# Performance work log

Hardware: AMD Instinct MI355X
Metric: run time of the kernel (lower is better)

Reference implementation:

```python
import jax, jax.numpy as jnp
import numpy as np

B, N, DIM = 4, 1024, 1024
H, DH = 16, 64
NUM_MEM = 4
TOPK = 64
QK_SCALE = 10.0  # qk_norm_scale


def l2norm(t, eps=1e-12):
    # qk_norm_groups == 1 -> normalize over full head dim
    return t / jnp.clip(jnp.linalg.norm(t, axis=-1, keepdims=True), eps)


def setup_inputs() -> dict:
    key = jax.random.key(0)
    ks = jax.random.split(key, 12)
    s = 0.02
    inp = {
        "x": jax.random.normal(ks[0], (B, N, DIM), dtype=jnp.float32),
        "Wq": jax.random.normal(ks[1], (DIM, H * DH), dtype=jnp.float32) * s,
        "Wk": jax.random.normal(ks[2], (DIM, H * DH), dtype=jnp.float32) * s,
        "Wv": jax.random.normal(ks[3], (DIM, H * DH), dtype=jnp.float32) * s,
        "W_pre_th": jax.random.normal(ks[4], (H, H), dtype=jnp.float32) * (1.0 / H) ** 0.5,
        "W_post_th": jax.random.normal(ks[5], (H, H), dtype=jnp.float32) * (1.0 / H) ** 0.5,
        "mem_k": jax.random.normal(ks[6], (H, NUM_MEM, DH), dtype=jnp.float32),
        "mem_v": jax.random.normal(ks[7], (H, NUM_MEM, DH), dtype=jnp.float32),
        "head_scale_params": jnp.ones((1, H, 1, 1), dtype=jnp.float32),
        "Wg": jax.random.normal(ks[8], (DIM, H * DH), dtype=jnp.float32) * s,
        "bg": jnp.ones((H * DH,), dtype=jnp.float32),
        "Wo": jax.random.normal(ks[9], (H * DH, DIM), dtype=jnp.float32) * s,
    }
    return inp


def reference(x, Wq, Wk, Wv, W_pre_th, W_post_th, mem_k, mem_v,
              head_scale_params, Wg, bg, Wo):
    b, n, _ = x.shape
    # projections -> b h n d
    q = (x @ Wq).reshape(b, n, H, DH).transpose(0, 2, 1, 3)
    k = (x @ Wk).reshape(b, n, H, DH).transpose(0, 2, 1, 3)
    v = (x @ Wv).reshape(b, n, H, DH).transpose(0, 2, 1, 3)

    # memory key/values prepended along the key axis
    mk = jnp.broadcast_to(mem_k[None], (b, H, NUM_MEM, DH))
    mv = jnp.broadcast_to(mem_v[None], (b, H, NUM_MEM, DH))
    k = jnp.concatenate([mk, k], axis=2)
    v = jnp.concatenate([mv, v], axis=2)

    # qk-norm: l2 normalize then fixed scale
    q = l2norm(q)
    k = l2norm(k)

    dots = jnp.einsum("bhid,bhjd->bhij", q, k) * QK_SCALE  # b h n (n+m)
    # pre-softmax talking heads (1x1 conv over head channels)
    dots = jnp.einsum("hg,bgij->bhij", W_pre_th, dots)

    mask_value = -jnp.finfo(dots.dtype).max
    j = n + NUM_MEM
    # causal mask, left-padded False over the memory columns
    col_pos = jnp.arange(j) - NUM_MEM  # mem cols get negative pos -> never masked
    causal = jnp.arange(n)[:, None] < col_pos[None, :]  # (n, j)
    dots = jnp.where(causal[None, None], mask_value, dots)

    # sparse top-k: keep only entries >= k-th largest per row
    top = jax.lax.top_k(dots, TOPK)[0]
    vk = top[..., -1:]
    dots = jnp.where(dots < vk, mask_value, dots)

    attn = jax.nn.softmax(dots, axis=-1)
    # post-softmax talking heads
    attn = jnp.einsum("hg,bgij->bhij", W_post_th, attn)

    out = jnp.einsum("bhij,bhjd->bhid", attn, v)
    out = out * head_scale_params
    out = out.transpose(0, 2, 1, 3).reshape(b, n, H * DH)

    gates = x @ Wg + bg
    out = out * jax.nn.sigmoid(gates)
    return out @ Wo
```

## Files before the change

### kernel.cpp

```cpp
#include <hip/hip_runtime.h>
#include <hip/hip_bf16.h>
#include <float.h>

#define B_ 4
#define N_ 1024
#define H_ 16
#define DH_ 64
#define NM_ 4
#define J_ 1028
#define IT_ 4
#define JST 1064
#define TOPK_ 64
#define QKSCALE 10.0f
#define KTF_BG 67584
#define VTF_DC 16896

typedef __attribute__((ext_vector_type(8))) short short8;
typedef __attribute__((ext_vector_type(4))) float f32x4;
typedef __attribute__((ext_vector_type(8))) unsigned short ushort8;
typedef __attribute__((ext_vector_type(4))) unsigned int u32x4;
typedef __attribute__((ext_vector_type(2))) unsigned int u32x2;
typedef _Float16 half8 __attribute__((ext_vector_type(8)));

__device__ __forceinline__ unsigned short f2b(float f){
  union { float f; unsigned int i; } c; c.f = f;
  unsigned int r = c.i + 0x7FFFu + ((c.i >> 16) & 1u);
  return (unsigned short)(r >> 16);
}
__device__ __forceinline__ unsigned short f2h(float f){
  return __builtin_bit_cast(unsigned short, (_Float16)f);
}
__device__ __forceinline__ float h2f(unsigned short u){
  return (float)__builtin_bit_cast(_Float16, u);
}
__device__ __forceinline__ unsigned int h2key(unsigned int u){
  return (u & 0x8000u) ? (~u & 0xFFFFu) : (u | 0x8000u);
}
__device__ __forceinline__ float key2f(unsigned int k){
  unsigned int u = (k & 0x8000u) ? (k & 0x7FFFu) : (~k & 0xFFFFu);
  return h2f((unsigned short)u);
}

__global__ void k_cvtAll(const float* __restrict__ x,  const float* __restrict__ wq,
                         const float* __restrict__ wk, const float* __restrict__ wv,
                         const float* __restrict__ wg, const float* __restrict__ wo,
                         unsigned short* __restrict__ xb, unsigned short* __restrict__ wcat,
                         unsigned short* __restrict__ wob,
                         const float* __restrict__ mk, const float* __restrict__ mv,
                         unsigned short* __restrict__ ktF, unsigned short* __restrict__ vtF){
  const int NX = 4096 * 1024, NW = 1024 * 1024;
  if (blockIdx.x >= 2044){
    int h = (blockIdx.x - 2044) * 4 + (threadIdx.x >> 6);
    int d = threadIdx.x & 63;
    unsigned short kh[4], vh[4];
    #pragma unroll
    for (int mm = 0; mm < 4; ++mm){
      float kv = mk[(h * 4 + mm) * 64 + d];
      float ss = kv * kv;
      #pragma unroll
      for (int off = 32; off; off >>= 1) ss += __shfl_xor(ss, off);
      kh[mm] = f2h(kv / fmaxf(sqrtf(ss), 1e-12f));
      vh[mm] = f2h(mv[(h * 4 + mm) * 64 + d]);
    }
    for (int b = 0; b < B_; ++b){
      int bg = b * 16 + h;
      #pragma unroll
      for (int mm = 0; mm < 4; ++mm)
        ktF[(size_t)bg * KTF_BG + (size_t)(d >> 5) * 512 + (mm + ((d >> 3) & 3) * 16) * 8 + (d & 7)] = kh[mm];
      #pragma unroll
      for (int mm = 0; mm < 4; ++mm)
        vtF[(size_t)bg * KTF_BG + (size_t)(d >> 4) * VTF_DC + (d & 15) * 8 + mm] = vh[mm];
      {
        unsigned int* kz = (unsigned int*)(ktF + (size_t)bg * KTF_BG + 64 * 1024);
        for (int c = d; c < 1024; c += 64) kz[c] = 0u;
      }
      #pragma unroll
      for (int dc = 0; dc < 4; ++dc){
        unsigned int* vz = (unsigned int*)(vtF + (size_t)bg * KTF_BG + (size_t)dc * VTF_DC + 32 * 512);
        for (int c = d; c < 256; c += 64) vz[c] = 0u;
      }
    }
    return;
  }
  int i = blockIdx.x * 256 + threadIdx.x;
  const int st = 2044 * 256;
  for (; i < NX + 5 * NW; i += st){
    if (i < NX){ xb[i] = f2b(x[i]); }
    else {
      int k = i - NX;
      int which = k >> 20, off = k & (NW - 1);
      if (which == 4){ wob[off] = f2b(wo[off]); }
      else {
        const float* s = which == 0 ? wq : which == 1 ? wk : which == 2 ? wv : wg;
        wcat[(size_t)(off >> 10) * 4096 + which * 1024 + (off & 1023)] = f2b(s[off]);
      }
    }
  }
}

__global__ __launch_bounds__(256) void k_gemmF(const unsigned short* __restrict__ A,
                                               const unsigned short* __restrict__ Wc,
                                               unsigned short* __restrict__ qn,
                                               unsigned short* __restrict__ ktF,
                                               unsigned short* __restrict__ vtF,
                                               unsigned short* __restrict__ gate,
                                               const float* __restrict__ bgv)
{
  __shared__ unsigned short As[128][72];
  __shared__ unsigned short Bs[64][72];
  const int t = threadIdx.x;
  const int m0 = blockIdx.y * 128, n0 = blockIdx.x * 64;
  const int l = t & 63, w = t >> 6;
  const int l15 = l & 15, l4 = l >> 4;

  f32x4 acc[2][4];
  #pragma unroll
  for (int a = 0; a < 2; ++a)
    #pragma unroll
    for (int b2 = 0; b2 < 4; ++b2) acc[a][b2] = (f32x4){0.f, 0.f, 0.f, 0.f};

  for (int k0 = 0; k0 < 1024; k0 += 64){
    #pragma unroll
    for (int cc = 0; cc < 4; ++cc){
      int c = t + cc * 256;
      int row = c >> 3, colc = (c & 7) * 8;
      *(ushort8*)&As[row][colc] = *(const ushort8*)&A[(m0 + row) * 1024 + k0 + colc];
    }
    #pragma unroll
    for (int cc = 0; cc < 2; ++cc){
      int c = t + cc * 256;
      int kk = c >> 3, nc = (c & 7) * 8;
      ushort8 vb = *(const ushort8*)&Wc[(size_t)(k0 + kk) * 4096 + n0 + nc];
      #pragma unroll
      for (int e = 0; e < 8; ++e) Bs[nc + e][kk] = vb[e];
    }
    __syncthreads();
    #pragma unroll
    for (int ks = 0; ks < 64; ks += 32){
      short8 af[2], bfr[4];
      #pragma unroll
      for (int mf = 0; mf < 2; ++mf) af[mf]  = *(const short8*)&As[w * 32 + mf * 16 + l15][ks + l4 * 8];
      #pragma unroll
      for (int nf = 0; nf < 4; ++nf) bfr[nf] = *(const short8*)&Bs[nf * 16 + l15][ks + l4 * 8];
      #pragma unroll
      for (int mf = 0; mf < 2; ++mf)
        #pragma unroll
        for (int nf = 0; nf < 4; ++nf)
          acc[mf][nf] = __builtin_amdgcn_mfma_f32_16x16x32_bf16(af[mf], bfr[nf], acc[mf][nf], 0, 0, 0);
    }
    __syncthreads();
  }

  const int which = n0 >> 10;
  const int ncol0 = n0 & 1023;
  const int hcol = ncol0 >> 6;
  #pragma unroll
  for (int mf = 0; mf < 2; ++mf){
    if (which == 2){
      int row0 = m0 + w * 32 + mf * 16 + l4 * 4;
      int bb = row0 >> 10;
      int j0 = (row0 & 1023) + NM_;
      int jtE = j0 >> 5, lj = (j0 & 31) >> 3, e0 = j0 & 7;
      #pragma unroll
      for (int nf = 0; nf < 4; ++nf){
        int col = ncol0 + nf * 16 + l15;
        int h = col >> 6, d = col & 63;
        unsigned int lo = (unsigned int)f2h(acc[mf][nf][0]) | ((unsigned int)f2h(acc[mf][nf][1]) << 16);
        unsigned int hi = (unsigned int)f2h(acc[mf][nf][2]) | ((unsigned int)f2h(acc[mf][nf][3]) << 16);
        unsigned short* dst = vtF + (size_t)(bb * 16 + h) * KTF_BG +
                              (size_t)(d >> 4) * VTF_DC + (size_t)jtE * 512 +
                              ((d & 15) + lj * 16) * 8 + e0;
        *(u32x2*)dst = (u32x2){lo, hi};
      }
    } else {
      #pragma unroll
      for (int r = 0; r < 4; ++r){
        int row = m0 + w * 32 + mf * 16 + l4 * 4 + r;
        float rn = 1.f;
        if (which <= 1){
          float ss = 0.f;
          #pragma unroll
          for (int nf = 0; nf < 4; ++nf) ss += acc[mf][nf][r] * acc[mf][nf][r];
          #pragma unroll
          for (int off = 1; off < 16; off <<= 1) ss += __shfl_xor(ss, off);
          rn = 1.f / fmaxf(sqrtf(ss), 1e-12f);
          if (which == 0) rn *= QKSCALE;
        }
        #pragma unroll
        for (int nf = 0; nf < 4; ++nf){
          int col = ncol0 + nf * 16 + l15;
          float v = acc[mf][nf][r];
          int bb = row >> 10, ii = row & 1023;
          if (which == 3){
            float g = v + bgv[3 * 1024 + col];
            gate[(size_t)row * 1024 + col] = f2h(1.f / (1.f + __expf(-g)));
          } else if (which == 0){
            int d = col & 63;
            qn[((size_t)(bb * H_ + hcol) * N_ + ii) * DH_ + d] = f2h(v * rn);
          } else {
            int j = ii + NM_;
            int d = col & 63;
            ktF[(size_t)(bb * 16 + hcol) * KTF_BG + (size_t)(j >> 4) * 1024 +
                (size_t)(d >> 5) * 512 + ((j & 15) + ((d >> 3) & 3) * 16) * 8 + (d & 7)]
              = f2h(v * rn);
          }
        }
      }
    }
  }
}

__global__ __launch_bounds__(256) void k_gemmO(const unsigned short* __restrict__ A,
                                               const unsigned short* __restrict__ W,
                                               float* __restrict__ outp)
{
  __shared__ unsigned short As[128][72];
  __shared__ unsigned short Bs[64][72];
  const int t = threadIdx.x;
  const int m0 = blockIdx.y * 128, n0 = blockIdx.x * 64;
  const int l = t & 63, w = t >> 6;
  const int l15 = l & 15, l4 = l >> 4;

  f32x4 acc[2][4];
  #pragma unroll
  for (int a = 0; a < 2; ++a)
    #pragma unroll
    for (int b2 = 0; b2 < 4; ++b2) acc[a][b2] = (f32x4){0.f, 0.f, 0.f, 0.f};

  for (int k0 = 0; k0 < 1024; k0 += 64){
    #pragma unroll
    for (int cc = 0; cc < 4; ++cc){
      int c = t + cc * 256;
      int row = c >> 3, colc = (c & 7) * 8;
      *(ushort8*)&As[row][colc] = *(const ushort8*)&A[(m0 + row) * 1024 + k0 + colc];
    }
    #pragma unroll
    for (int cc = 0; cc < 2; ++cc){
      int c = t + cc * 256;
      int kk = c >> 3, nc = (c & 7) * 8;
      ushort8 vb = *(const ushort8*)&W[(size_t)(k0 + kk) * 1024 + n0 + nc];
      #pragma unroll
      for (int e = 0; e < 8; ++e) Bs[nc + e][kk] = vb[e];
    }
    __syncthreads();
    #pragma unroll
    for (int ks = 0; ks < 64; ks += 32){
      short8 af[2], bfr[4];
      #pragma unroll
      for (int mf = 0; mf < 2; ++mf) af[mf]  = *(const short8*)&As[w * 32 + mf * 16 + l15][ks + l4 * 8];
      #pragma unroll
      for (int nf = 0; nf < 4; ++nf) bfr[nf] = *(const short8*)&Bs[nf * 16 + l15][ks + l4 * 8];
      #pragma unroll
      for (int mf = 0; mf < 2; ++mf)
        #pragma unroll
        for (int nf = 0; nf < 4; ++nf)
          acc[mf][nf] = __builtin_amdgcn_mfma_f32_16x16x32_bf16(af[mf], bfr[nf], acc[mf][nf], 0, 0, 0);
    }
    __syncthreads();
  }

  #pragma unroll
  for (int mf = 0; mf < 2; ++mf)
    #pragma unroll
    for (int r = 0; r < 4; ++r){
      int row = m0 + w * 32 + mf * 16 + l4 * 4 + r;
      #pragma unroll
      for (int nf = 0; nf < 4; ++nf)
        outp[(size_t)row * 1024 + n0 + nf * 16 + l15] = acc[mf][nf][r];
    }
}

__global__ __launch_bounds__(1024) void k_attnM(
  const unsigned short* __restrict__ qn, const unsigned short* __restrict__ ktF,
  const unsigned short* __restrict__ vtF, const float* __restrict__ wpre,
  const float* __restrict__ wpost, const float* __restrict__ hsc,
  const unsigned short* __restrict__ gate, unsigned short* __restrict__ aout)
{
  __shared__ unsigned short sd[16 * IT_ * JST];
  __shared__ unsigned short qls[16 * 4 * 64];
  __shared__ unsigned short wpre16[16 * 32];
  __shared__ unsigned short wpost16[16 * 32];

  const int blk = blockIdx.x;
  const int b = (blk >> 1) & 3;
  const int idx = ((blk >> 3) << 1) | (blk & 1);
  const int rd = idx >> 6, jj = idx & 63;
  const int it = (rd == 0) ? (255 - jj) : (rd == 1) ? (128 + jj) : (rd == 2) ? (127 - jj) : jj;
  const int i0 = it * IT_;
  const int nAmax = i0 + IT_ + 4;
  const int nJtA = (nAmax + 15) >> 4;
  const int nJtE = (nAmax + 31) >> 5;
  const int nJtD = nJtE * 2;
  const int jc = nJtE * 32;
  const int t = threadIdx.x;
  const int w = t >> 6, l = t & 63;
  const int l15 = l & 15, l4 = l >> 4;

  if (t < 256){
    int h = t >> 4, g = t & 15;
    wpre16[h * 32 + g]       = f2h(wpre[h * 16 + g]);
    wpre16[h * 32 + 16 + g]  = 0;
    wpost16[h * 32 + g]      = f2h(wpost[h * 16 + g]);
    wpost16[h * 32 + 16 + g] = 0;
  }
  for (int c = t; c < 2048; c += 1024){
    int d2 = c & 31, ii = (c >> 5) & 3, g = c >> 7;
    ((unsigned int*)qls)[c] =
      *(const unsigned int*)(qn + ((size_t)(b * 16 + g) * N_ + i0 + ii) * 64 + d2 * 2);
  }
  __syncthreads();

  {
    const int nw16 = (nJtA > w) ? ((nJtA - w + 15) >> 4) : 0;
    const int ntask = nw16 * 16;
    if (ntask > 0){
      const int tmax = ntask - 1;
      const unsigned short* kl = ktF + (size_t)(b * 16) * KTF_BG + (size_t)l * 8;
      auto kp = [&](int task)->const unsigned short*{
        int tt = task > tmax ? tmax : task;
        int g = tt & 15, jti = tt >> 4;
        return kl + (size_t)g * KTF_BG + (((size_t)(w + jti * 16)) << 10);
      };
      const unsigned short* p0 = kp(0);
      const unsigned short* p1 = kp(1);
      half8 kA0 = *(const half8*)p0, kA1 = *(const half8*)(p0 + 512);
      half8 kB0 = *(const half8*)p1, kB1 = *(const half8*)(p1 + 512);
      for (int task = 0; task < ntask; task += 2){
        half8 cA0 = kA0, cA1 = kA1, cB0 = kB0, cB1 = kB1;
        const unsigned short* pa = kp(task + 2);
        const unsigned short* pb = kp(task + 3);
        kA0 = *(const half8*)pa; kA1 = *(const half8*)(pa + 512);
        kB0 = *(const half8*)pb; kB1 = *(const half8*)(pb + 512);
        #pragma unroll
        for (int s = 0; s < 2; ++s){
          const int tt = task + s;
          const int g = tt & 15, jt = w + ((tt >> 4) << 4);
          const unsigned short* qp = &qls[(g * 4 + (l15 & 3)) * 64 + l4 * 8];
          half8 qf0 = *(const half8*)(qp);
          half8 qf1 = *(const half8*)(qp + 32);
          f32x4 acc = (f32x4){0.f, 0.f, 0.f, 0.f};
          acc = __builtin_amdgcn_mfma_f32_16x16x32_f16(s ? cB0 : cA0, qf0, acc, 0, 0, 0);
          acc = __builtin_amdgcn_mfma_f32_16x16x32_f16(s ? cB1 : cA1, qf1, acc, 0, 0, 0);
          if (l15 < IT_){
            unsigned int pk0 = (unsigned int)f2h(acc[0]) | ((unsigned int)f2h(acc[1]) << 16);
            unsigned int pk1 = (unsigned int)f2h(acc[2]) | ((unsigned int)f2h(acc[3]) << 16);
            unsigned int* dst = (unsigned int*)&sd[(g * IT_ + l15) * JST + jt * 16 + l4 * 4];
            dst[0] = pk0; dst[1] = pk1;
          }
        }
      }
    }
  }
  __syncthreads();

  {
    half8 wa = *(const half8*)&wpre16[l15 * 32 + l4 * 8];
    const int ntask = IT_ * nJtA;
    for (int task = w; task < ntask; task += 16){
      const int ii = task & (IT_ - 1), jt = task >> 2;
      unsigned int fb[4] = {0u, 0u, 0u, 0u};
      if (l4 < 2){
        const unsigned short* src = &sd[((l4 * 8) * IT_ + ii) * JST + jt * 16 + l15];
        #pragma unroll
        for (int e = 0; e < 8; e += 2){
          unsigned int lo = src[(size_t)(e)     * IT_ * JST];
          unsigned int hi = src[(size_t)(e + 1) * IT_ * JST];
          fb[e >> 1] = (lo & 0xFFFFu) | (hi << 16);
        }
      }
      f32x4 acc = (f32x4){0.f, 0.f, 0.f, 0.f};
      acc = __builtin_amdgcn_mfma_f32_16x16x32_f16(wa, __builtin_bit_cast(half8, *(u32x4*)fb), acc, 0, 0, 0);
      #pragma unroll
      for (int r = 0; r < 4; ++r)
        sd[((l4 * 4 + r) * IT_ + ii) * JST + jt * 16 + l15] = f2h(acc[r]);
    }
  }
  __syncthreads();

  for (int rr = 0; rr < 4; ++rr){
    const int row = w * 4 + rr;
    const int g = row >> 2, ii = row & 3;
    const int nA = i0 + ii + 5;
    unsigned short* rowp = &sd[(g * IT_ + ii) * JST];
    unsigned int kw[9];
    #pragma unroll
    for (int grp = 0; grp < 9; ++grp){
      kw[grp] = 0u;
      if (grp * 128 < jc){
        int j = grp * 128 + l * 2;
        unsigned int u = (j < JST) ? *(const unsigned int*)(rowp + j) : 0u;
        unsigned int klo = h2key(u & 0xFFFFu);
        unsigned int khi = h2key(u >> 16);
        if (j     >= nA) klo = 0u;
        if (j + 1 >= nA) khi = 0u;
        kw[grp] = klo | (khi << 16);
      }
    }
    unsigned int kmx = 0u;
    #pragma unroll
    for (int grp = 0; grp < 9; ++grp){
      if (grp * 128 < jc){
        unsigned int m2 = max(kw[grp] >> 16, kw[grp] & 0xFFFFu);
        kmx = max(kmx, m2);
      }
    }
    #pragma unroll
    for (int off = 32; off; off >>= 1) kmx = max(kmx, (unsigned int)__shfl_xor((int)kmx, off));
    const float mx = key2f(kmx);

    unsigned int T = 0u;
    if (nA > TOPK_){
      for (int bit = 15; bit >= 2; --bit){
        unsigned int Tc = T | (1u << bit);
        int c = 0;
        #pragma unroll
        for (int grp = 0; grp < 9; ++grp){
          if (grp * 128 < jc){
            c += __popcll(__ballot((kw[grp] & 0xFFFFu) >= Tc));
            c += __popcll(__ballot((kw[grp] >> 16) >= Tc));
          }
        }
        if (c >= TOPK_){
          T = Tc;
          if (c == TOPK_) break;
        }
      }
    }
    if (T == 0u) T = 1u;

    float s = 0.f;
    float ev[18];
    #pragma unroll
    for (int grp = 0; grp < 9; ++grp){
      if (grp * 128 < jc){
        unsigned int klo = kw[grp] & 0xFFFFu, khi = kw[grp] >> 16;
        float elo = (klo >= T) ? __expf(key2f(klo) - mx) : 0.f;
        float ehi = (khi >= T) ? __expf(key2f(khi) - mx) : 0.f;
        ev[grp * 2] = elo; ev[grp * 2 + 1] = ehi;
        s += elo + ehi;
      }
    }
    #pragma unroll
    for (int off = 32; off; off >>= 1) s += __shfl_xor(s, off);
    float inv = 1.f / s;
    #pragma unroll
    for (int grp = 0; grp < 9; ++grp){
      if (grp * 128 < jc){
        int j = grp * 128 + l * 2;
        if (j < JST)
          *(unsigned int*)(rowp + j) =
            (unsigned int)f2h(ev[grp * 2] * inv) | ((unsigned int)f2h(ev[grp * 2 + 1] * inv) << 16);
      }
    }
  }
  __syncthreads();

  {
    const int ntask = IT_ * nJtD;
    for (int task = w; task < ntask; task += 16){
      const int ii = task & (IT_ - 1), jt = task >> 2;
      half8 wa = *(const half8*)&wpost16[l15 * 32 + l4 * 8];
      unsigned int fb[4] = {0u, 0u, 0u, 0u};
      if (l4 < 2){
        const unsigned short* src = &sd[((l4 * 8) * IT_ + ii) * JST + jt * 16 + l15];
        #pragma unroll
        for (int e = 0; e < 8; e += 2){
          unsigned int lo = src[(size_t)(e)     * IT_ * JST];
          unsigned int hi = src[(size_t)(e + 1) * IT_ * JST];
          fb[e >> 1] = (lo & 0xFFFFu) | (hi << 16);
        }
      }
      f32x4 acc = (f32x4){0.f, 0.f, 0.f, 0.f};
      acc = __builtin_amdgcn_mfma_f32_16x16x32_f16(wa, __builtin_bit_cast(half8, *(u32x4*)fb), acc, 0, 0, 0);
      #pragma unroll
      for (int r = 0; r < 4; ++r)
        sd[((l4 * 4 + r) * IT_ + ii) * JST + jt * 16 + l15] = f2h(acc[r]);
    }
  }
  __syncthreads();

  for (int task = w; task < 64; task += 16){
    const int h = task >> 2, dc = task & 3;
    const int bg = b * 16 + h;
    const unsigned short* vbase = vtF + (size_t)bg * KTF_BG + (size_t)dc * VTF_DC + (size_t)l * 8;
    const unsigned short* arow = &sd[(h * IT_ + (l15 & 3)) * JST + l4 * 8];
    const int jm = nJtE - 1;
    auto vp_ = [&](int jt)->const half8*{
      int tt = jt > jm ? jm : jt;
      return (const half8*)(vbase + ((size_t)tt << 9));
    };
    half8 vA = *vp_(0), vB = *vp_(1);
    f32x4 acc = (f32x4){0.f, 0.f, 0.f, 0.f};
    int jt = 0;
    for (; jt + 2 <= nJtE; jt += 2){
      half8 cA = vA, cB = vB;
      vA = *vp_(jt + 2); vB = *vp_(jt + 3);
      half8 af0 = *(const half8*)(arow + jt * 32);
      half8 af1 = *(const half8*)(arow + jt * 32 + 32);
      acc = __builtin_amdgcn_mfma_f32_16x16x32_f16(af0, cA, acc, 0, 0, 0);
      acc = __builtin_amdgcn_mfma_f32_16x16x32_f16(af1, cB, acc, 0, 0, 0);
    }
    if (jt < nJtE){
      half8 af0 = *(const half8*)(arow + jt * 32);
      acc = __builtin_amdgcn_mfma_f32_16x16x32_f16(af0, vA, acc, 0, 0, 0);
    }
    if (l4 == 0){
      const float hs = hsc[h];
      #pragma unroll
      for (int r = 0; r < IT_; ++r){
        const int irow = (b << 10) | (i0 + r);
        const size_t o = (size_t)irow * 1024 + h * 64 + dc * 16 + l15;
        aout[o] = f2b(acc[r] * hs * h2f(gate[o]));
      }
    }
  }
}

extern "C" void kernel_launch(void* const* d_in, const int* in_sizes, int n_in,
                              void* d_out, int out_size, void* d_ws, size_t ws_size,
                              hipStream_t stream) {
  const float* x     = (const float*)d_in[0];
  const float* Wq    = (const float*)d_in[1];
  const float* Wk    = (const float*)d_in[2];
  const float* Wv    = (const float*)d_in[3];
  const float* Wpre  = (const float*)d_in[4];
  const float* Wpost = (const float*)d_in[5];
  const float* mk    = (const float*)d_in[6];
  const float* mv    = (const float*)d_in[7];
  const float* hsc   = (const float*)d_in[8];
  const float* Wg    = (const float*)d_in[9];
  const float* bg    = (const float*)d_in[10];
  const float* Wo    = (const float*)d_in[11];
  float* out = (float*)d_out;

  char* ws = (char*)d_ws;
  size_t off = 0;
  auto alloc = [&](size_t bytes) -> void* {
    void* p = ws + off; off += (bytes + 255) & ~(size_t)255; return p;
  };
  unsigned short* xb   = (unsigned short*)alloc((size_t)4096 * 1024 * 2);
  unsigned short* wcat = (unsigned short*)alloc((size_t)1024 * 4096 * 2);
  unsigned short* wob  = (unsigned short*)alloc((size_t)1024 * 1024 * 2);
  unsigned short* qn   = (unsigned short*)alloc((size_t)B_ * H_ * N_ * DH_ * 2);
  unsigned short* ktF  = (unsigned short*)alloc((size_t)B_ * H_ * KTF_BG * 2);
  unsigned short* vtF  = (unsigned short*)alloc((size_t)B_ * H_ * KTF_BG * 2);
  unsigned short* gate = (unsigned short*)alloc((size_t)4096 * 1024 * 2);
  unsigned short* aout = (unsigned short*)alloc((size_t)4096 * 1024 * 2);

  k_cvtAll<<<2048, 256, 0, stream>>>(x, Wq, Wk, Wv, Wg, Wo, xb, wcat, wob,
                                     mk, mv, ktF, vtF);

  k_gemmF<<<dim3(64, 32), 256, 0, stream>>>(xb, wcat, qn, ktF, vtF, gate, bg - 3 * 1024);

  k_attnM<<<1024, 1024, 0, stream>>>(qn, ktF, vtF, Wpre, Wpost, hsc, gate, aout);

  k_gemmO<<<dim3(16, 32), 256, 0, stream>>>(aout, wob, out);
}
```

Baseline: 360.2 us.

## Pre-transpose weights in conversion kernel and split attention by causal length

The conversion kernel now writes the projection and output weights transposed (N-major), using an LDS tile transpose. The GEMMs can then load B tiles with vectorized row copies instead of scattered per-element transposed LDS stores. Attention is split into two launches templated on the maximum key-tile count, so the late-row half and early-row half each size their shared score buffer and top-k loops to their causal extent. The shorter half uses less LDS, which may allow more blocks per CU. The cost is a second kernel launch and a more complex conversion kernel.

```diff
diff --git a/kernel.cpp b/kernel.cpp
--- a/kernel.cpp
+++ b/kernel.cpp
@@ -9,7 +9,6 @@
 #define NM_ 4
 #define J_ 1028
 #define IT_ 4
-#define JST 1064
 #define TOPK_ 64
 #define QKSCALE 10.0f
 #define KTF_BG 67584
@@ -41,17 +40,48 @@
   return h2f((unsigned short)u);
 }
 
-__global__ void k_cvtAll(const float* __restrict__ x,  const float* __restrict__ wq,
-                         const float* __restrict__ wk, const float* __restrict__ wv,
-                         const float* __restrict__ wg, const float* __restrict__ wo,
-                         unsigned short* __restrict__ xb, unsigned short* __restrict__ wcat,
-                         unsigned short* __restrict__ wob,
-                         const float* __restrict__ mk, const float* __restrict__ mv,
-                         unsigned short* __restrict__ ktF, unsigned short* __restrict__ vtF){
-  const int NX = 4096 * 1024, NW = 1024 * 1024;
-  if (blockIdx.x >= 2044){
-    int h = (blockIdx.x - 2044) * 4 + (threadIdx.x >> 6);
-    int d = threadIdx.x & 63;
+__global__ __launch_bounds__(256) void k_cvtAll(
+    const float* __restrict__ x,  const float* __restrict__ wq,
+    const float* __restrict__ wk, const float* __restrict__ wv,
+    const float* __restrict__ wg, const float* __restrict__ wo,
+    unsigned short* __restrict__ xb, unsigned short* __restrict__ wcatT,
+    unsigned short* __restrict__ wobT,
+    const float* __restrict__ mk, const float* __restrict__ mv,
+    unsigned short* __restrict__ ktF, unsigned short* __restrict__ vtF){
+  const int t = threadIdx.x;
+  const unsigned bid = blockIdx.x;
+  if (bid < 1280){
+    __shared__ unsigned short tile[64][70];
+    const int which = bid >> 8;
+    const int tl = bid & 255;
+    const int tr = tl >> 4, tc = tl & 15;
+    const float* src = which == 0 ? wq : which == 1 ? wk : which == 2 ? wv : which == 3 ? wg : wo;
+    {
+      int r = t >> 2, c0 = (t & 3) * 16;
+      const float* sp = src + (size_t)(tr * 64 + r) * 1024 + tc * 64 + c0;
+      #pragma unroll
+      for (int e = 0; e < 16; ++e) tile[r][c0 + e] = f2b(sp[e]);
+    }
+    __syncthreads();
+    {
+      int rn = t >> 2, k0 = (t & 3) * 16;
+      int n = tc * 64 + rn;
+      unsigned short* dp = (which == 4)
+        ? wobT + (size_t)n * 1024 + tr * 64 + k0
+        : wcatT + ((size_t)which * 1024 + n) * 1024 + tr * 64 + k0;
+      ushort8 v0, v1;
+      #pragma unroll
+      for (int e = 0; e < 8; ++e) v0[e] = tile[k0 + e][rn];
+      #pragma unroll
+      for (int e = 0; e < 8; ++e) v1[e] = tile[k0 + 8 + e][rn];
+      *(ushort8*)dp = v0;
+      *(ushort8*)(dp + 8) = v1;
+    }
+    return;
+  }
+  if (bid >= 1280 && bid < 1284){
+    int h = (bid - 1280) * 4 + (t >> 6);
+    int d = t & 63;
     unsigned short kh[4], vh[4];
     #pragma unroll
     for (int mm = 0; mm < 4; ++mm){
@@ -82,24 +112,13 @@
     }
     return;
   }
-  int i = blockIdx.x * 256 + threadIdx.x;
-  const int st = 2044 * 256;
-  for (; i < NX + 5 * NW; i += st){
-    if (i < NX){ xb[i] = f2b(x[i]); }
-    else {
-      int k = i - NX;
-      int which = k >> 20, off = k & (NW - 1);
-      if (which == 4){ wob[off] = f2b(wo[off]); }
-      else {
-        const float* s = which == 0 ? wq : which == 1 ? wk : which == 2 ? wv : wg;
-        wcat[(size_t)(off >> 10) * 4096 + which * 1024 + (off & 1023)] = f2b(s[off]);
-      }
-    }
-  }
+  int i = (bid - 1284) * 256 + t;
+  const int st = (3072 - 1284) * 256;
+  for (; i < 4096 * 1024; i += st) xb[i] = f2b(x[i]);
 }
 
 __global__ __launch_bounds__(256) void k_gemmF(const unsigned short* __restrict__ A,
-                                               const unsigned short* __restrict__ Wc,
+                                               const unsigned short* __restrict__ WcT,
                                                unsigned short* __restrict__ qn,
                                                unsigned short* __restrict__ ktF,
                                                unsigned short* __restrict__ vtF,
@@ -129,10 +148,8 @@
     #pragma unroll
     for (int cc = 0; cc < 2; ++cc){
       int c = t + cc * 256;
-      int kk = c >> 3, nc = (c & 7) * 8;
-      ushort8 vb = *(const ushort8*)&Wc[(size_t)(k0 + kk) * 4096 + n0 + nc];
-      #pragma unroll
-      for (int e = 0; e < 8; ++e) Bs[nc + e][kk] = vb[e];
+      int row = c >> 3, colc = (c & 7) * 8;
+      *(ushort8*)&Bs[row][colc] = *(const ushort8*)&WcT[(size_t)(n0 + row) * 1024 + k0 + colc];
     }
     __syncthreads();
     #pragma unroll
@@ -211,7 +228,7 @@
 }
 
 __global__ __launch_bounds__(256) void k_gemmO(const unsigned short* __restrict__ A,
-                                               const unsigned short* __restrict__ W,
+                                               const unsigned short* __restrict__ WT,
                                                float* __restrict__ outp)
 {
   __shared__ unsigned short As[128][72];
@@ -237,10 +254,8 @@
     #pragma unroll
     for (int cc = 0; cc < 2; ++cc){
       int c = t + cc * 256;
-      int kk = c >> 3, nc = (c & 7) * 8;
-      ushort8 vb = *(const ushort8*)&W[(size_t)(k0 + kk) * 1024 + n0 + nc];
-      #pragma unroll
-      for (int e = 0; e < 8; ++e) Bs[nc + e][kk] = vb[e];
+      int row = c >> 3, colc = (c & 7) * 8;
+      *(ushort8*)&Bs[row][colc] = *(const ushort8*)&WT[(size_t)(n0 + row) * 1024 + k0 + colc];
     }
     __syncthreads();
     #pragma unroll
@@ -270,13 +285,17 @@
     }
 }
 
+template<int NJTE_MAX>
 __global__ __launch_bounds__(1024) void k_attnM(
   const unsigned short* __restrict__ qn, const unsigned short* __restrict__ ktF,
   const unsigned short* __restrict__ vtF, const float* __restrict__ wpre,
   const float* __restrict__ wpost, const float* __restrict__ hsc,
-  const unsigned short* __restrict__ gate, unsigned short* __restrict__ aout)
+  const unsigned short* __restrict__ gate, unsigned short* __restrict__ aout,
+  int itBase)
 {
-  __shared__ unsigned short sd[16 * IT_ * JST];
+  constexpr int JSTT = NJTE_MAX * 32 + 8;
+  constexpr int NG = (JSTT + 127) / 128;
+  __shared__ unsigned short sd[16 * IT_ * JSTT];
   __shared__ unsigned short qls[16 * 4 * 64];
   __shared__ unsigned short wpre16[16 * 32];
   __shared__ unsigned short wpost16[16 * 32];
@@ -284,8 +303,7 @@
   const int blk = blockIdx.x;
   const int b = (blk >> 1) & 3;
   const int idx = ((blk >> 3) << 1) | (blk & 1);
-  const int rd = idx >> 6, jj = idx & 63;
-  const int it = (rd == 0) ? (255 - jj) : (rd == 1) ? (128 + jj) : (rd == 2) ? (127 - jj) : jj;
+  const int it = itBase - idx;
   const int i0 = it * IT_;
   const int nAmax = i0 + IT_ + 4;
   const int nJtA = (nAmax + 15) >> 4;
@@ -344,7 +362,7 @@
           if (l15 < IT_){
             unsigned int pk0 = (unsigned int)f2h(acc[0]) | ((unsigned int)f2h(acc[1]) << 16);
             unsigned int pk1 = (unsigned int)f2h(acc[2]) | ((unsigned int)f2h(acc[3]) << 16);
-            unsigned int* dst = (unsigned int*)&sd[(g * IT_ + l15) * JST + jt * 16 + l4 * 4];
+            unsigned int* dst = (unsigned int*)&sd[(g * IT_ + l15) * JSTT + jt * 16 + l4 * 4];
             dst[0] = pk0; dst[1] = pk1;
           }
         }
@@ -360,11 +378,11 @@
       const int ii = task & (IT_ - 1), jt = task >> 2;
       unsigned int fb[4] = {0u, 0u, 0u, 0u};
       if (l4 < 2){
-        const unsigned short* src = &sd[((l4 * 8) * IT_ + ii) * JST + jt * 16 + l15];
+        const unsigned short* src = &sd[((l4 * 8) * IT_ + ii) * JSTT + jt * 16 + l15];
         #pragma unroll
         for (int e = 0; e < 8; e += 2){
-          unsigned int lo = src[(size_t)(e)     * IT_ * JST];
-          unsigned int hi = src[(size_t)(e + 1) * IT_ * JST];
+          unsigned int lo = src[(size_t)(e)     * IT_ * JSTT];
+          unsigned int hi = src[(size_t)(e + 1) * IT_ * JSTT];
           fb[e >> 1] = (lo & 0xFFFFu) | (hi << 16);
         }
       }
@@ -372,7 +390,7 @@
       acc = __builtin_amdgcn_mfma_f32_16x16x32_f16(wa, __builtin_bit_cast(half8, *(u32x4*)fb), acc, 0, 0, 0);
       #pragma unroll
       for (int r = 0; r < 4; ++r)
-        sd[((l4 * 4 + r) * IT_ + ii) * JST + jt * 16 + l15] = f2h(acc[r]);
+        sd[((l4 * 4 + r) * IT_ + ii) * JSTT + jt * 16 + l15] = f2h(acc[r]);
     }
   }
   __syncthreads();
@@ -381,14 +399,14 @@
     const int row = w * 4 + rr;
     const int g = row >> 2, ii = row & 3;
     const int nA = i0 + ii + 5;
-    unsigned short* rowp = &sd[(g * IT_ + ii) * JST];
-    unsigned int kw[9];
-    #pragma unroll
-    for (int grp = 0; grp < 9; ++grp){
+    unsigned short* rowp = &sd[(g * IT_ + ii) * JSTT];
+    unsigned int kw[NG];
+    #pragma unroll
+    for (int grp = 0; grp < NG; ++grp){
       kw[grp] = 0u;
       if (grp * 128 < jc){
         int j = grp * 128 + l * 2;
-        unsigned int u = (j < JST) ? *(const unsigned int*)(rowp + j) : 0u;
+        unsigned int u = (j < JSTT) ? *(const unsigned int*)(rowp + j) : 0u;
         unsigned int klo = h2key(u & 0xFFFFu);
         unsigned int khi = h2key(u >> 16);
         if (j     >= nA) klo = 0u;
@@ -398,7 +416,7 @@
     }
     unsigned int kmx = 0u;
     #pragma unroll
-    for (int grp = 0; grp < 9; ++grp){
+    for (int grp = 0; grp < NG; ++grp){
       if (grp * 128 < jc){
         unsigned int m2 = max(kw[grp] >> 16, kw[grp] & 0xFFFFu);
         kmx = max(kmx, m2);
@@ -414,7 +432,7 @@
         unsigned int Tc = T | (1u << bit);
         int c = 0;
         #pragma unroll
-        for (int grp = 0; grp < 9; ++grp){
+        for (int grp = 0; grp < NG; ++grp){
           if (grp * 128 < jc){
             c += __popcll(__ballot((kw[grp] & 0xFFFFu) >= Tc));
             c += __popcll(__ballot((kw[grp] >> 16) >= Tc));
@@ -429,9 +447,9 @@
     if (T == 0u) T = 1u;
 
     float s = 0.f;
-    float ev[18];
-    #pragma unroll
-    for (int grp = 0; grp < 9; ++grp){
+    float ev[2 * NG];
+    #pragma unroll
+    for (int grp = 0; grp < NG; ++grp){
       if (grp * 128 < jc){
         unsigned int klo = kw[grp] & 0xFFFFu, khi = kw[grp] >> 16;
         float elo = (klo >= T) ? __expf(key2f(klo) - mx) : 0.f;
@@ -444,10 +462,10 @@
     for (int off = 32; off; off >>= 1) s += __shfl_xor(s, off);
     float inv = 1.f / s;
     #pragma unroll
-    for (int grp = 0; grp < 9; ++grp){
+    for (int grp = 0; grp < NG; ++grp){
       if (grp * 128 < jc){
         int j = grp * 128 + l * 2;
-        if (j < JST)
+        if (j < JSTT)
           *(unsigned int*)(rowp + j) =
             (unsigned int)f2h(ev[grp * 2] * inv) | ((unsigned int)f2h(ev[grp * 2 + 1] * inv) << 16);
       }
@@ -462,11 +480,11 @@
       half8 wa = *(const half8*)&wpost16[l15 * 32 + l4 * 8];
       unsigned int fb[4] = {0u, 0u, 0u, 0u};
       if (l4 < 2){
-        const unsigned short* src = &sd[((l4 * 8) * IT_ + ii) * JST + jt * 16 + l15];
+        const unsigned short* src = &sd[((l4 * 8) * IT_ + ii) * JSTT + jt * 16 + l15];
         #pragma unroll
         for (int e = 0; e < 8; e += 2){
-          unsigned int lo = src[(size_t)(e)     * IT_ * JST];
-          unsigned int hi = src[(size_t)(e + 1) * IT_ * JST];
+          unsigned int lo = src[(size_t)(e)     * IT_ * JSTT];
+          unsigned int hi = src[(size_t)(e + 1) * IT_ * JSTT];
           fb[e >> 1] = (lo & 0xFFFFu) | (hi << 16);
         }
       }
@@ -474,7 +492,7 @@
       acc = __builtin_amdgcn_mfma_f32_16x16x32_f16(wa, __builtin_bit_cast(half8, *(u32x4*)fb), acc, 0, 0, 0);
       #pragma unroll
       for (int r = 0; r < 4; ++r)
-        sd[((l4 * 4 + r) * IT_ + ii) * JST + jt * 16 + l15] = f2h(acc[r]);
+        sd[((l4 * 4 + r) * IT_ + ii) * JSTT + jt * 16 + l15] = f2h(acc[r]);
     }
   }
   __syncthreads();
@@ -483,7 +501,7 @@
     const int h = task >> 2, dc = task & 3;
     const int bg = b * 16 + h;
     const unsigned short* vbase = vtF + (size_t)bg * KTF_BG + (size_t)dc * VTF_DC + (size_t)l * 8;
-    const unsigned short* arow = &sd[(h * IT_ + (l15 & 3)) * JST + l4 * 8];
+    const unsigned short* arow = &sd[(h * IT_ + (l15 & 3)) * JSTT + l4 * 8];
     const int jm = nJtE - 1;
     auto vp_ = [&](int jt)->const half8*{
       int tt = jt > jm ? jm : jt;
@@ -538,21 +556,22 @@
   auto alloc = [&](size_t bytes) -> void* {
     void* p = ws + off; off += (bytes + 255) & ~(size_t)255; return p;
   };
-  unsigned short* xb   = (unsigned short*)alloc((size_t)4096 * 1024 * 2);
-  unsigned short* wcat = (unsigned short*)alloc((size_t)1024 * 4096 * 2);
-  unsigned short* wob  = (unsigned short*)alloc((size_t)1024 * 1024 * 2);
-  unsigned short* qn   = (unsigned short*)alloc((size_t)B_ * H_ * N_ * DH_ * 2);
-  unsigned short* ktF  = (unsigned short*)alloc((size_t)B_ * H_ * KTF_BG * 2);
-  unsigned short* vtF  = (unsigned short*)alloc((size_t)B_ * H_ * KTF_BG * 2);
-  unsigned short* gate = (unsigned short*)alloc((size_t)4096 * 1024 * 2);
-  unsigned short* aout = (unsigned short*)alloc((size_t)4096 * 1024 * 2);
-
-  k_cvtAll<<<2048, 256, 0, stream>>>(x, Wq, Wk, Wv, Wg, Wo, xb, wcat, wob,
+  unsigned short* xb    = (unsigned short*)alloc((size_t)4096 * 1024 * 2);
+  unsigned short* wcatT = (unsigned short*)alloc((size_t)4096 * 1024 * 2);
+  unsigned short* wobT  = (unsigned short*)alloc((size_t)1024 * 1024 * 2);
+  unsigned short* qn    = (unsigned short*)alloc((size_t)B_ * H_ * N_ * DH_ * 2);
+  unsigned short* ktF   = (unsigned short*)alloc((size_t)B_ * H_ * KTF_BG * 2);
+  unsigned short* vtF   = (unsigned short*)alloc((size_t)B_ * H_ * KTF_BG * 2);
+  unsigned short* gate  = (unsigned short*)alloc((size_t)4096 * 1024 * 2);
+  unsigned short* aout  = (unsigned short*)alloc((size_t)4096 * 1024 * 2);
+
+  k_cvtAll<<<3072, 256, 0, stream>>>(x, Wq, Wk, Wv, Wg, Wo, xb, wcatT, wobT,
                                      mk, mv, ktF, vtF);
 
-  k_gemmF<<<dim3(64, 32), 256, 0, stream>>>(xb, wcat, qn, ktF, vtF, gate, bg - 3 * 1024);
-
-  k_attnM<<<1024, 1024, 0, stream>>>(qn, ktF, vtF, Wpre, Wpost, hsc, gate, aout);
-
-  k_gemmO<<<dim3(16, 32), 256, 0, stream>>>(aout, wob, out);
-}
+  k_gemmF<<<dim3(64, 32), 256, 0, stream>>>(xb, wcatT, qn, ktF, vtF, gate, bg - 3 * 1024);
+
+  k_attnM<33><<<512, 1024, 0, stream>>>(qn, ktF, vtF, Wpre, Wpost, hsc, gate, aout, 255);
+  k_attnM<17><<<512, 1024, 0, stream>>>(qn, ktF, vtF, Wpre, Wpost, hsc, gate, aout, 127);
+
+  k_gemmO<<<dim3(16, 32), 256, 0, stream>>>(aout, wobT, out);
+}
```

Result: faster. 318.6 us (-11.5%).
